# Performance work log

Hardware: AMD Instinct MI355X
Metric: run time of the kernel (lower is better)

## Reference

```python
import math
import jax, jax.numpy as jnp
import numpy as np

BSZ, N_HEADS, N_KV_HEADS, SEQLEN, HEAD_DIM = 1, 32, 8, 2048, 128
DIM = N_HEADS * HEAD_DIM  # 4096
N_REP = N_HEADS // N_KV_HEADS  # 4
NEG = -1e9


def setup_inputs() -> dict:
    key = jax.random.key(0)
    kq, kk, kv = jax.random.split(key, 3)
    q = jax.random.normal(kq, (BSZ, N_HEADS, SEQLEN, HEAD_DIM), dtype=jnp.float32)
    k = jax.random.normal(kk, (BSZ, N_KV_HEADS, SEQLEN, HEAD_DIM), dtype=jnp.float32)
    v = jax.random.normal(kv, (BSZ, N_KV_HEADS, SEQLEN, HEAD_DIM), dtype=jnp.float32)
    # additive causal mask: 0 on/below diagonal, large negative above
    causal = jnp.tril(jnp.ones((SEQLEN, SEQLEN), dtype=bool))
    mask = jnp.where(causal, 0.0, NEG).astype(jnp.float32)
    input_pos = jnp.zeros((1,), dtype=jnp.int64)
    return {"input_pos": input_pos, "q": q, "k": k, "v": v,
            "bsz": BSZ, "seqlen": SEQLEN, "mask": mask}


def reference(input_pos, q, k, v, bsz, seqlen, mask):
    # repeat_kv: (b, n_kv, s, d) -> (b, n_kv*n_rep, s, d), repeat_interleave on head dim
    k = jnp.repeat(k, N_REP, axis=1)
    v = jnp.repeat(v, N_REP, axis=1)
    scale = 1.0 / math.sqrt(q.shape[-1])
    # (b, h, s, s)
    attn = jnp.einsum("bhqd,bhkd->bhqk", q, k) * scale + mask
    attn = jax.nn.softmax(attn, axis=-1)
    y = jnp.einsum("bhqk,bhkd->bhqd", attn, v)  # (b, h, s, d)
    return y.transpose(0, 2, 1, 3).reshape(bsz, seqlen, DIM)
```

## Files before the change

kernel.cpp:

```cpp
#include <hip/hip_runtime.h>
#include <hip/hip_bf16.h>

#define SEQ 2048
#define HD 128
#define NH 32
#define NKV 8
#define ODIM 4096
#define QB 64
#define KVB 64
#define SCALE 0.08838834764831845f
#define SCALE_L2E 0.12752767f
#define NEGBIG -1e9f
#define NEGBIG_L2 -1.4426950e9f
#define THR_L2 11.54f

typedef __attribute__((ext_vector_type(8))) short bf16x8;
typedef __attribute__((ext_vector_type(4))) float f32x4;

__device__ __forceinline__ unsigned short f2bf(float x) {
  union { __hip_bfloat16 b; unsigned short u; } c;
  c.b = __float2bfloat16(x);
  return c.u;
}

__device__ __forceinline__ unsigned pack2bf(float lo, float hi) {
  union { __hip_bfloat162 h; unsigned u; } c;
  c.h = __float22bfloat162_rn(float2{lo, hi});
  return c.u;
}

__device__ __forceinline__ void gload_lds16(const unsigned char* g, unsigned char* l) {
  __builtin_amdgcn_global_load_lds(
      (const __attribute__((address_space(1))) void*)g,
      (__attribute__((address_space(3))) void*)l, 16, 0, 0);
}

#define KWORK (NKV * SEQ * 16)
#define VWORK (NKV * (SEQ / 2) * 16)
__global__ __launch_bounds__(256) void sdpa_prepass(
    const float* __restrict__ k, const float* __restrict__ v,
    unsigned char* __restrict__ ws) {
  unsigned char* kimg = ws;
  unsigned char* vimg = ws + (NKV * 32 * 16384);
  int idx = (int)blockIdx.x * 256 + (int)threadIdx.x;
  if (idx < KWORK) {
    int hkv = idx >> 15;
    int rem = idx & 32767;
    int rg = rem >> 4;
    int c8 = (rem & 15) << 3;
    const float* src = k + ((size_t)hkv * SEQ + rg) * HD + c8;
    float4 a = *(const float4*)(src);
    float4 b = *(const float4*)(src + 4);
    union { unsigned short hh[8]; uint4 u4; } pk;
    pk.hh[0]=f2bf(a.x); pk.hh[1]=f2bf(a.y); pk.hh[2]=f2bf(a.z); pk.hh[3]=f2bf(a.w);
    pk.hh[4]=f2bf(b.x); pk.hh[5]=f2bf(b.y); pk.hh[6]=f2bf(b.z); pk.hh[7]=f2bf(b.w);
    int t = rg >> 6, r = rg & 63;
    size_t base = ((size_t)(hkv * 32 + t)) << 14;
    *(uint4*)(kimg + base + (r << 8) + ((c8 << 1) ^ ((r & 7) << 4))) = pk.u4;
  } else {
    int u = idx - KWORK;
    if (u >= VWORK) return;
    int hkv = u >> 14;
    int rem = u & 16383;
    int pr = rem >> 4;
    int d0 = (rem & 15) << 3;
    int rg = pr << 1;
    const float* s0 = v + ((size_t)hkv * SEQ + rg) * HD + d0;
    const float* s1 = s0 + HD;
    float4 a0 = *(const float4*)(s0);
    float4 b0 = *(const float4*)(s0 + 4);
    float4 a1 = *(const float4*)(s1);
    float4 b1 = *(const float4*)(s1 + 4);
    float lo[8] = {a0.x,a0.y,a0.z,a0.w,b0.x,b0.y,b0.z,b0.w};
    float hi[8] = {a1.x,a1.y,a1.z,a1.w,b1.x,b1.y,b1.z,b1.w};
    int t = rg >> 6, rr = rg & 63;
    size_t base = ((size_t)(hkv * 32 + t)) << 14;
    int rb = rr << 1;
    #pragma unroll
    for (int j = 0; j < 8; ++j) {
      int d = d0 + j;
      *(unsigned*)(vimg + base + (d << 7) + (rb ^ ((d & 7) << 4))) =
          pack2bf(lo[j], hi[j]);
    }
  }
}

__global__ __launch_bounds__(512, 4) void sdpa_flash_kernel(
    const float* __restrict__ q, const unsigned char* __restrict__ kimg,
    const unsigned char* __restrict__ vimg, float* __restrict__ out) {
  __shared__ __align__(16) unsigned char smem[49152];
  const int tid = threadIdx.x;
  const int w = tid >> 6;
  const int l = tid & 63;
  const int lm = l & 15;
  const int lg = l >> 4;

  const int p = (int)blockIdx.x;
  const int qtA = p;
  const int qtB = 31 - p;
  const int myqt = (w < 4) ? qtA : qtB;
  const int h = (int)blockIdx.y;
  const int hkv = h >> 2;
  const int qbase = myqt * QB + 16 * (w & 3);
  const int myrow = qbase + lm;

  bf16x8 qa[4];
  {
    const float* qr = q + ((size_t)(h * SEQ + myrow)) * HD + 8 * lg;
    #pragma unroll
    for (int c = 0; c < 4; ++c) {
      float4 a = *(const float4*)(qr + 32 * c);
      float4 b = *(const float4*)(qr + 32 * c + 4);
      union { unsigned short hh[8]; bf16x8 vv; } pk;
      pk.hh[0] = f2bf(a.x * SCALE_L2E); pk.hh[1] = f2bf(a.y * SCALE_L2E);
      pk.hh[2] = f2bf(a.z * SCALE_L2E); pk.hh[3] = f2bf(a.w * SCALE_L2E);
      pk.hh[4] = f2bf(b.x * SCALE_L2E); pk.hh[5] = f2bf(b.y * SCALE_L2E);
      pk.hh[6] = f2bf(b.z * SCALE_L2E); pk.hh[7] = f2bf(b.w * SCALE_L2E);
      qa[c] = pk.vv;
    }
  }

  f32x4 o[8];
  #pragma unroll
  for (int i = 0; i < 8; ++i) o[i] = (f32x4){0.f, 0.f, 0.f, 0.f};
  float mrow = -1e30f;
  float lrow = 0.f;

  const int ntiles = qtB + 1;
  const unsigned char* kt0 = kimg + (((size_t)(hkv * 32)) << 14);
  const unsigned char* vt0 = vimg + (((size_t)(hkv * 32)) << 14);
  const int woff = w << 10;

#define STAGE_K(tt, Kb) {                                                    \
    const unsigned char* ks_ = kt0 + (((size_t)(tt)) << 14);                 \
    gload_lds16(ks_ + woff + (l << 4), (Kb) + woff);                         \
    gload_lds16(ks_ + 8192 + woff + (l << 4), (Kb) + 8192 + woff);           \
  }
#define STAGE_V(tt, Vb) {                                                    \
    const unsigned char* vs_ = vt0 + (((size_t)(tt)) << 14);                 \
    gload_lds16(vs_ + woff + (l << 4), (Vb) + woff);                         \
    gload_lds16(vs_ + 8192 + woff + (l << 4), (Vb) + 8192 + woff);           \
  }

  unsigned char* sA = smem;
  unsigned char* sB = smem + 16384;
  unsigned char* sC = smem + 32768;

  STAGE_K(0, sA);
  STAGE_V(0, sB);
  __syncthreads();

  for (int t = 0; t < ntiles; ++t) {
    const int kv0 = t * KVB;
    const bool have_next = (t + 1 < ntiles);
    if (have_next) STAGE_K(t + 1, sC);

    const bool act = (t <= myqt);
    bf16x8 pb[2];
    if (act) {
      f32x4 s[4];
      #pragma unroll
      for (int nt = 0; nt < 4; ++nt) s[nt] = (f32x4){0.f, 0.f, 0.f, 0.f};
      __builtin_amdgcn_s_setprio(1);
      #pragma unroll
      for (int nt = 0; nt < 4; ++nt) {
        int r = (nt << 4) + lm;
        #pragma unroll
        for (int kc = 0; kc < 4; ++kc) {
          int byte = (r << 8) + (((kc << 6) + (lg << 4)) ^ ((r & 7) << 4));
          bf16x8 kb = *(const bf16x8*)(sA + byte);
          s[nt] = __builtin_amdgcn_mfma_f32_16x16x32_bf16(kb, qa[kc], s[nt], 0, 0, 0);
        }
      }
      __builtin_amdgcn_s_setprio(0);

      if (kv0 + KVB - 1 > qbase) {
        #pragma unroll
        for (int nt = 0; nt < 4; ++nt) {
          #pragma unroll
          for (int i = 0; i < 4; ++i) {
            int col = kv0 + (nt << 4) + (lg << 2) + i;
            s[nt][i] += (col > myrow) ? NEGBIG_L2 : 0.f;
          }
        }
      }

      float tm = -1e30f;
      #pragma unroll
      for (int nt = 0; nt < 4; ++nt)
        #pragma unroll
        for (int i = 0; i < 4; ++i) tm = fmaxf(tm, s[nt][i]);
      tm = fmaxf(tm, __shfl_xor(tm, 16));
      tm = fmaxf(tm, __shfl_xor(tm, 32));
      if (!__all(tm <= mrow + THR_L2)) {
        float mn = fmaxf(mrow, tm);
        float fac = __builtin_amdgcn_exp2f(mrow - mn);
        mrow = mn;
        lrow *= fac;
        #pragma unroll
        for (int nt2 = 0; nt2 < 8; ++nt2) {
          #pragma unroll
          for (int i = 0; i < 4; ++i) o[nt2][i] *= fac;
        }
      }
      float rs = 0.f;
      #pragma unroll
      for (int nt = 0; nt < 4; ++nt) {
        #pragma unroll
        for (int i = 0; i < 4; ++i) {
          float pv = __builtin_amdgcn_exp2f(s[nt][i] - mrow);
          s[nt][i] = pv;
          rs += pv;
        }
      }
      rs += __shfl_xor(rs, 16);
      rs += __shfl_xor(rs, 32);
      lrow += rs;

      unsigned pk0[4], pk1[4];
      #pragma unroll
      for (int nt = 0; nt < 4; ++nt) {
        pk0[nt] = pack2bf(s[nt][0], s[nt][1]);
        pk1[nt] = pack2bf(s[nt][2], s[nt][3]);
      }
      const int srcA = lm + ((lg & 1) << 5);
      const int srcB = srcA + 16;
      const bool lo2 = (lg < 2);
      #pragma unroll
      for (int kc = 0; kc < 2; ++kc) {
        int a0 = __shfl((int)pk0[2*kc], srcA), b0 = __shfl((int)pk0[2*kc+1], srcA);
        int a1 = __shfl((int)pk1[2*kc], srcA), b1 = __shfl((int)pk1[2*kc+1], srcA);
        int a2 = __shfl((int)pk0[2*kc], srcB), b2 = __shfl((int)pk0[2*kc+1], srcB);
        int a3 = __shfl((int)pk1[2*kc], srcB), b3 = __shfl((int)pk1[2*kc+1], srcB);
        union { int uu[4]; bf16x8 v; } pw;
        pw.uu[0] = lo2 ? a0 : b0;
        pw.uu[1] = lo2 ? a1 : b1;
        pw.uu[2] = lo2 ? a2 : b2;
        pw.uu[3] = lo2 ? a3 : b3;
        pb[kc] = pw.v;
      }
    }

    __syncthreads();
    if (have_next) STAGE_V(t + 1, sA);

    if (act) {
      __builtin_amdgcn_s_setprio(1);
      #pragma unroll
      for (int nt2 = 0; nt2 < 8; ++nt2) {
        int dr = (nt2 << 4) + lm;
        #pragma unroll
        for (int kc = 0; kc < 2; ++kc) {
          int byte = (dr << 7) + (((kc << 6) + (lg << 4)) ^ ((dr & 7) << 4));
          bf16x8 vb = *(const bf16x8*)(sB + byte);
          o[nt2] = __builtin_amdgcn_mfma_f32_16x16x32_bf16(vb, pb[kc], o[nt2], 0, 0, 0);
        }
      }
      __builtin_amdgcn_s_setprio(0);
    }

    __syncthreads();
    unsigned char* nA = sC;
    unsigned char* nB = sA;
    unsigned char* nC = sB;
    sA = nA; sB = nB; sC = nC;
  }

  float inv = 1.f / lrow;
  float* orow = out + (size_t)myrow * ODIM + h * HD + (lg << 2);
  #pragma unroll
  for (int nt2 = 0; nt2 < 8; ++nt2) {
    float4 st = {o[nt2][0] * inv, o[nt2][1] * inv, o[nt2][2] * inv, o[nt2][3] * inv};
    *(float4*)(orow + (nt2 << 4)) = st;
  }
#undef STAGE_K
#undef STAGE_V
}

__global__ __launch_bounds__(512, 4) void sdpa_flash_fb(
    const float* __restrict__ q, const float* __restrict__ k,
    const float* __restrict__ v, float* __restrict__ out) {
  __shared__ __align__(16) unsigned char smem[65536];
  const int tid = threadIdx.x;
  const int w = tid >> 6;
  const int l = tid & 63;
  const int lm = l & 15;
  const int lg = l >> 4;
  const int p = (int)blockIdx.x;
  const int qtA = p;
  const int qtB = 31 - p;
  const int myqt = (w < 4) ? qtA : qtB;
  const int h = (int)blockIdx.y;
  const int hkv = h >> 2;
  const int qbase = myqt * QB + 16 * (w & 3);
  const int myrow = qbase + lm;
  bf16x8 qa[4];
  {
    const float* qr = q + ((size_t)(h * SEQ + myrow)) * HD + 8 * lg;
    #pragma unroll
    for (int c = 0; c < 4; ++c) {
      float4 a = *(const float4*)(qr + 32 * c);
      float4 b = *(const float4*)(qr + 32 * c + 4);
      union { unsigned short hh[8]; bf16x8 vv; } pk;
      pk.hh[0] = f2bf(a.x * SCALE); pk.hh[1] = f2bf(a.y * SCALE);
      pk.hh[2] = f2bf(a.z * SCALE); pk.hh[3] = f2bf(a.w * SCALE);
      pk.hh[4] = f2bf(b.x * SCALE); pk.hh[5] = f2bf(b.y * SCALE);
      pk.hh[6] = f2bf(b.z * SCALE); pk.hh[7] = f2bf(b.w * SCALE);
      qa[c] = pk.vv;
    }
  }
  f32x4 o[8];
  #pragma unroll
  for (int i = 0; i < 8; ++i) o[i] = (f32x4){0.f, 0.f, 0.f, 0.f};
  float mrow = -1e30f;
  float lrow = 0.f;
  const int ntiles = qtB + 1;
  const float* kg0 = k + (size_t)hkv * SEQ * HD;
  const float* vg0 = v + (size_t)hkv * SEQ * HD;
  const int k_r0 = tid >> 4;
  const int k_c8 = (tid & 15) << 3;
  const int v_rr = (tid & 31) << 1;
  const int v_d0 = (tid >> 5) << 3;
  float4 ka0, kb0, ka1, kb1, va0, vb0, va1, vb1;
#define LOADT(tt) {                                                          \
    const float* kg_ = kg0 + (size_t)((tt) * KVB) * HD + k_r0 * HD + k_c8;   \
    ka0 = *(const float4*)(kg_);                                             \
    kb0 = *(const float4*)(kg_ + 4);                                         \
    ka1 = *(const float4*)(kg_ + 32 * HD);                                   \
    kb1 = *(const float4*)(kg_ + 32 * HD + 4);                               \
    const float* vg_ = vg0 + (size_t)((tt) * KVB) * HD + v_rr * HD + v_d0;   \
    va0 = *(const float4*)(vg_);                                             \
    vb0 = *(const float4*)(vg_ + 4);                                         \
    va1 = *(const float4*)(vg_ + HD);                                        \
    vb1 = *(const float4*)(vg_ + HD + 4);                                    \
  }
#define WRITELDS(bufbase) {                                                  \
    unsigned char* Kb_ = (bufbase);                                          \
    unsigned char* Vb_ = (bufbase) + 16384;                                  \
    {                                                                        \
      union { unsigned short hh[8]; uint4 u4; } pk_;                         \
      pk_.hh[0]=f2bf(ka0.x); pk_.hh[1]=f2bf(ka0.y);                          \
      pk_.hh[2]=f2bf(ka0.z); pk_.hh[3]=f2bf(ka0.w);                          \
      pk_.hh[4]=f2bf(kb0.x); pk_.hh[5]=f2bf(kb0.y);                          \
      pk_.hh[6]=f2bf(kb0.z); pk_.hh[7]=f2bf(kb0.w);                          \
      int byte_ = (k_r0 << 8) + ((k_c8 << 1) ^ ((k_r0 & 7) << 4));           \
      *(uint4*)(Kb_ + byte_) = pk_.u4;                                       \
    }                                                                        \
    {                                                                        \
      int r1_ = k_r0 + 32;                                                   \
      union { unsigned short hh[8]; uint4 u4; } pk_;                         \
      pk_.hh[0]=f2bf(ka1.x); pk_.hh[1]=f2bf(ka1.y);                          \
      pk_.hh[2]=f2bf(ka1.z); pk_.hh[3]=f2bf(ka1.w);                          \
      pk_.hh[4]=f2bf(kb1.x); pk_.hh[5]=f2bf(kb1.y);                          \
      pk_.hh[6]=f2bf(kb1.z); pk_.hh[7]=f2bf(kb1.w);                          \
      int byte_ = (r1_ << 8) + ((k_c8 << 1) ^ ((r1_ & 7) << 4));             \
      *(uint4*)(Kb_ + byte_) = pk_.u4;                                       \
    }                                                                        \
    {                                                                        \
      unsigned w0_ = pack2bf(va0.x, va1.x), w1_ = pack2bf(va0.y, va1.y);     \
      unsigned w2_ = pack2bf(va0.z, va1.z), w3_ = pack2bf(va0.w, va1.w);     \
      unsigned w4_ = pack2bf(vb0.x, vb1.x), w5_ = pack2bf(vb0.y, vb1.y);     \
      unsigned w6_ = pack2bf(vb0.z, vb1.z), w7_ = pack2bf(vb0.w, vb1.w);     \
      int rb_ = v_rr << 1;                                                   \
      int d_;                                                                \
      d_ = v_d0;     *(unsigned*)(Vb_ + (d_ << 7) + (rb_ ^ ((d_ & 7) << 4))) = w0_; \
      d_ = v_d0 + 1; *(unsigned*)(Vb_ + (d_ << 7) + (rb_ ^ ((d_ & 7) << 4))) = w1_; \
      d_ = v_d0 + 2; *(unsigned*)(Vb_ + (d_ << 7) + (rb_ ^ ((d_ & 7) << 4))) = w2_; \
      d_ = v_d0 + 3; *(unsigned*)(Vb_ + (d_ << 7) + (rb_ ^ ((d_ & 7) << 4))) = w3_; \
      d_ = v_d0 + 4; *(unsigned*)(Vb_ + (d_ << 7) + (rb_ ^ ((d_ & 7) << 4))) = w4_; \
      d_ = v_d0 + 5; *(unsigned*)(Vb_ + (d_ << 7) + (rb_ ^ ((d_ & 7) << 4))) = w5_; \
      d_ = v_d0 + 6; *(unsigned*)(Vb_ + (d_ << 7) + (rb_ ^ ((d_ & 7) << 4))) = w6_; \
      d_ = v_d0 + 7; *(unsigned*)(Vb_ + (d_ << 7) + (rb_ ^ ((d_ & 7) << 4))) = w7_; \
    }                                                                        \
  }
  LOADT(0);
  WRITELDS(smem);
  __syncthreads();
  int cur = 0;
  for (int t = 0; t < ntiles; ++t) {
    const int kv0 = t * KVB;
    const bool have_next = (t + 1 < ntiles);
    if (have_next) LOADT(t + 1);
    unsigned char* Klds = smem + (cur << 15);
    unsigned char* Vlds = Klds + 16384;
    if (t <= myqt) {
      f32x4 s[4];
      #pragma unroll
      for (int nt = 0; nt < 4; ++nt) s[nt] = (f32x4){0.f, 0.f, 0.f, 0.f};
      #pragma unroll
      for (int nt = 0; nt < 4; ++nt) {
        int r = (nt << 4) + lm;
        #pragma unroll
        for (int kc = 0; kc < 4; ++kc) {
          int byte = (r << 8) + (((kc << 6) + (lg << 4)) ^ ((r & 7) << 4));
          bf16x8 kb = *(const bf16x8*)(Klds + byte);
          s[nt] = __builtin_amdgcn_mfma_f32_16x16x32_bf16(kb, qa[kc], s[nt], 0, 0, 0);
        }
      }
      if (kv0 + KVB - 1 > qbase) {
        #pragma unroll
        for (int nt = 0; nt < 4; ++nt) {
          #pragma unroll
          for (int i = 0; i < 4; ++i) {
            int col = kv0 + (nt << 4) + (lg << 2) + i;
            s[nt][i] += (col > myrow) ? NEGBIG : 0.f;
          }
        }
      }
      float tm = -1e30f;
      #pragma unroll
      for (int nt = 0; nt < 4; ++nt)
        #pragma unroll
        for (int i = 0; i < 4; ++i) tm = fmaxf(tm, s[nt][i]);
      tm = fmaxf(tm, __shfl_xor(tm, 16));
      tm = fmaxf(tm, __shfl_xor(tm, 32));
      float mn = fmaxf(mrow, tm);
      float fac = __expf(mrow - mn);
      mrow = mn;
      float rs = 0.f;
      #pragma unroll
      for (int nt = 0; nt < 4; ++nt) {
        #pragma unroll
        for (int i = 0; i < 4; ++i) {
          float pv = __expf(s[nt][i] - mn);
          s[nt][i] = pv;
          rs += pv;
        }
      }
      rs += __shfl_xor(rs, 16);
      rs += __shfl_xor(rs, 32);
      lrow = lrow * fac + rs;
      #pragma unroll
      for (int nt2 = 0; nt2 < 8; ++nt2) {
        #pragma unroll
        for (int i = 0; i < 4; ++i) o[nt2][i] *= fac;
      }
      unsigned pk0[4], pk1[4];
      #pragma unroll
      for (int nt = 0; nt < 4; ++nt) {
        pk0[nt] = pack2bf(s[nt][0], s[nt][1]);
        pk1[nt] = pack2bf(s[nt][2], s[nt][3]);
      }
      const int srcA = lm + ((lg & 1) << 5);
      const int srcB = srcA + 16;
      const bool lo2 = (lg < 2);
      bf16x8 pb[2];
      #pragma unroll
      for (int kc = 0; kc < 2; ++kc) {
        int a0 = __shfl((int)pk0[2*kc], srcA), b0 = __shfl((int)pk0[2*kc+1], srcA);
        int a1 = __shfl((int)pk1[2*kc], srcA), b1 = __shfl((int)pk1[2*kc+1], srcA);
        int a2 = __shfl((int)pk0[2*kc], srcB), b2 = __shfl((int)pk0[2*kc+1], srcB);
        int a3 = __shfl((int)pk1[2*kc], srcB), b3 = __shfl((int)pk1[2*kc+1], srcB);
        union { int uu[4]; bf16x8 v; } pw;
        pw.uu[0] = lo2 ? a0 : b0;
        pw.uu[1] = lo2 ? a1 : b1;
        pw.uu[2] = lo2 ? a2 : b2;
        pw.uu[3] = lo2 ? a3 : b3;
        pb[kc] = pw.v;
      }
      #pragma unroll
      for (int nt2 = 0; nt2 < 8; ++nt2) {
        int dr = (nt2 << 4) + lm;
        #pragma unroll
        for (int kc = 0; kc < 2; ++kc) {
          int byte = (dr << 7) + (((kc << 6) + (lg << 4)) ^ ((dr & 7) << 4));
          bf16x8 vb = *(const bf16x8*)(Vlds + byte);
          o[nt2] = __builtin_amdgcn_mfma_f32_16x16x32_bf16(vb, pb[kc], o[nt2], 0, 0, 0);
        }
      }
    }
    if (have_next) {
      WRITELDS(smem + ((cur ^ 1) << 15));
    }
    __syncthreads();
    cur ^= 1;
  }
  float inv = 1.f / lrow;
  float* orow = out + (size_t)myrow * ODIM + h * HD + (lg << 2);
  #pragma unroll
  for (int nt2 = 0; nt2 < 8; ++nt2) {
    float4 st = {o[nt2][0] * inv, o[nt2][1] * inv, o[nt2][2] * inv, o[nt2][3] * inv};
    *(float4*)(orow + (nt2 << 4)) = st;
  }
#undef LOADT
#undef WRITELDS
}

extern "C" void kernel_launch(void* const* d_in, const int* in_sizes, int n_in,
                              void* d_out, int out_size, void* d_ws, size_t ws_size,
                              hipStream_t stream) {
  const float* q = (const float*)d_in[1];
  const float* k = (const float*)d_in[2];
  const float* v = (const float*)d_in[3];
  float* out = (float*)d_out;
  dim3 grid(SEQ / QB / 2, NH);
  const size_t need = (size_t)(NKV * 32 * 16384) * 2;
  if (ws_size >= need && d_ws != nullptr) {
    unsigned char* ws = (unsigned char*)d_ws;
    int total = KWORK + VWORK;
    sdpa_prepass<<<(total + 255) / 256, 256, 0, stream>>>(k, v, ws);
    sdpa_flash_kernel<<<grid, 512, 0, stream>>>(
        q, ws, ws + (NKV * 32 * 16384), out);
  } else {
    sdpa_flash_fb<<<grid, 512, 0, stream>>>(q, k, v, out);
  }
}
```

Measured before the change: 82.67 us.

## Have each wave process both paired query tiles, halving block size to 256 threads

Each block previously used 8 waves, with 4 waves on query tile A and 4 on the mirrored tile B. Now 4 waves each handle 16 rows from both tiles. Every K/V fragment read from LDS feeds two MFMAs, which halves LDS read traffic per MFMA and removes the load imbalance where tile-A waves idled on later iterations. The cost is double the accumulator and Q registers per thread, lower launch bounds (256,2) with possibly fewer resident waves, and each wave issuing 4 async copies per stage instead of 2.

```diff
diff --git a/kernel.cpp b/kernel.cpp
--- a/kernel.cpp
+++ b/kernel.cpp
@@ -85,7 +85,7 @@
   }
 }
 
-__global__ __launch_bounds__(512, 4) void sdpa_flash_kernel(
+__global__ __launch_bounds__(256, 2) void sdpa_flash_kernel(
     const float* __restrict__ q, const unsigned char* __restrict__ kimg,
     const unsigned char* __restrict__ vimg, float* __restrict__ out) {
   __shared__ __align__(16) unsigned char smem[49152];
@@ -98,48 +98,61 @@
   const int p = (int)blockIdx.x;
   const int qtA = p;
   const int qtB = 31 - p;
-  const int myqt = (w < 4) ? qtA : qtB;
   const int h = (int)blockIdx.y;
   const int hkv = h >> 2;
-  const int qbase = myqt * QB + 16 * (w & 3);
-  const int myrow = qbase + lm;
-
-  bf16x8 qa[4];
+  const int qbaseA = qtA * QB + 16 * w;
+  const int qbaseB = qtB * QB + 16 * w;
+  const int rowA = qbaseA + lm;
+  const int rowB = qbaseB + lm;
+
+  bf16x8 qa[2][4];
   {
-    const float* qr = q + ((size_t)(h * SEQ + myrow)) * HD + 8 * lg;
+    const int rows2[2] = {rowA, rowB};
     #pragma unroll
-    for (int c = 0; c < 4; ++c) {
-      float4 a = *(const float4*)(qr + 32 * c);
-      float4 b = *(const float4*)(qr + 32 * c + 4);
-      union { unsigned short hh[8]; bf16x8 vv; } pk;
-      pk.hh[0] = f2bf(a.x * SCALE_L2E); pk.hh[1] = f2bf(a.y * SCALE_L2E);
-      pk.hh[2] = f2bf(a.z * SCALE_L2E); pk.hh[3] = f2bf(a.w * SCALE_L2E);
-      pk.hh[4] = f2bf(b.x * SCALE_L2E); pk.hh[5] = f2bf(b.y * SCALE_L2E);
-      pk.hh[6] = f2bf(b.z * SCALE_L2E); pk.hh[7] = f2bf(b.w * SCALE_L2E);
-      qa[c] = pk.vv;
-    }
-  }
-
-  f32x4 o[8];
+    for (int u = 0; u < 2; ++u) {
+      const float* qr = q + ((size_t)(h * SEQ + rows2[u])) * HD + 8 * lg;
+      #pragma unroll
+      for (int c = 0; c < 4; ++c) {
+        float4 a = *(const float4*)(qr + 32 * c);
+        float4 b = *(const float4*)(qr + 32 * c + 4);
+        union { unsigned short hh[8]; bf16x8 vv; } pk;
+        pk.hh[0] = f2bf(a.x * SCALE_L2E); pk.hh[1] = f2bf(a.y * SCALE_L2E);
+        pk.hh[2] = f2bf(a.z * SCALE_L2E); pk.hh[3] = f2bf(a.w * SCALE_L2E);
+        pk.hh[4] = f2bf(b.x * SCALE_L2E); pk.hh[5] = f2bf(b.y * SCALE_L2E);
+        pk.hh[6] = f2bf(b.z * SCALE_L2E); pk.hh[7] = f2bf(b.w * SCALE_L2E);
+        qa[u][c] = pk.vv;
+      }
+    }
+  }
+
+  f32x4 o[2][8];
   #pragma unroll
-  for (int i = 0; i < 8; ++i) o[i] = (f32x4){0.f, 0.f, 0.f, 0.f};
-  float mrow = -1e30f;
-  float lrow = 0.f;
+  for (int u = 0; u < 2; ++u)
+    #pragma unroll
+    for (int i = 0; i < 8; ++i) o[u][i] = (f32x4){0.f, 0.f, 0.f, 0.f};
+  float mrow[2] = {-1e30f, -1e30f};
+  float lrow[2] = {0.f, 0.f};
 
   const int ntiles = qtB + 1;
   const unsigned char* kt0 = kimg + (((size_t)(hkv * 32)) << 14);
   const unsigned char* vt0 = vimg + (((size_t)(hkv * 32)) << 14);
-  const int woff = w << 10;
+  const int woff = w << 12;
 
 #define STAGE_K(tt, Kb) {                                                    \
-    const unsigned char* ks_ = kt0 + (((size_t)(tt)) << 14);                 \
-    gload_lds16(ks_ + woff + (l << 4), (Kb) + woff);                         \
-    gload_lds16(ks_ + 8192 + woff + (l << 4), (Kb) + 8192 + woff);           \
+    const unsigned char* ks_ = kt0 + (((size_t)(tt)) << 14) + woff + (l << 4); \
+    unsigned char* kd_ = (Kb) + woff;                                        \
+    gload_lds16(ks_, kd_);                                                   \
+    gload_lds16(ks_ + 1024, kd_ + 1024);                                     \
+    gload_lds16(ks_ + 2048, kd_ + 2048);                                     \
+    gload_lds16(ks_ + 3072, kd_ + 3072);                                     \
   }
 #define STAGE_V(tt, Vb) {                                                    \
-    const unsigned char* vs_ = vt0 + (((size_t)(tt)) << 14);                 \
-    gload_lds16(vs_ + woff + (l << 4), (Vb) + woff);                         \
-    gload_lds16(vs_ + 8192 + woff + (l << 4), (Vb) + 8192 + woff);           \
+    const unsigned char* vs_ = vt0 + (((size_t)(tt)) << 14) + woff + (l << 4); \
+    unsigned char* vd_ = (Vb) + woff;                                        \
+    gload_lds16(vs_, vd_);                                                   \
+    gload_lds16(vs_ + 1024, vd_ + 1024);                                     \
+    gload_lds16(vs_ + 2048, vd_ + 2048);                                     \
+    gload_lds16(vs_ + 3072, vd_ + 3072);                                     \
   }
 
   unsigned char* sA = smem;
@@ -155,12 +168,16 @@
     const bool have_next = (t + 1 < ntiles);
     if (have_next) STAGE_K(t + 1, sC);
 
-    const bool act = (t <= myqt);
-    bf16x8 pb[2];
-    if (act) {
-      f32x4 s[4];
-      #pragma unroll
-      for (int nt = 0; nt < 4; ++nt) s[nt] = (f32x4){0.f, 0.f, 0.f, 0.f};
+    const bool actA = (t <= qtA);
+    f32x4 s[2][4];
+    bf16x8 pb[2][2];
+
+    if (actA) {
+      #pragma unroll
+      for (int nt = 0; nt < 4; ++nt) {
+        s[0][nt] = (f32x4){0.f, 0.f, 0.f, 0.f};
+        s[1][nt] = (f32x4){0.f, 0.f, 0.f, 0.f};
+      }
       __builtin_amdgcn_s_setprio(1);
       #pragma unroll
       for (int nt = 0; nt < 4; ++nt) {
@@ -169,59 +186,86 @@
         for (int kc = 0; kc < 4; ++kc) {
           int byte = (r << 8) + (((kc << 6) + (lg << 4)) ^ ((r & 7) << 4));
           bf16x8 kb = *(const bf16x8*)(sA + byte);
-          s[nt] = __builtin_amdgcn_mfma_f32_16x16x32_bf16(kb, qa[kc], s[nt], 0, 0, 0);
+          s[0][nt] = __builtin_amdgcn_mfma_f32_16x16x32_bf16(kb, qa[0][kc], s[0][nt], 0, 0, 0);
+          s[1][nt] = __builtin_amdgcn_mfma_f32_16x16x32_bf16(kb, qa[1][kc], s[1][nt], 0, 0, 0);
         }
       }
       __builtin_amdgcn_s_setprio(0);
-
-      if (kv0 + KVB - 1 > qbase) {
-        #pragma unroll
-        for (int nt = 0; nt < 4; ++nt) {
-          #pragma unroll
-          for (int i = 0; i < 4; ++i) {
-            int col = kv0 + (nt << 4) + (lg << 2) + i;
-            s[nt][i] += (col > myrow) ? NEGBIG_L2 : 0.f;
-          }
-        }
-      }
-
+    } else {
+      #pragma unroll
+      for (int nt = 0; nt < 4; ++nt) s[1][nt] = (f32x4){0.f, 0.f, 0.f, 0.f};
+      __builtin_amdgcn_s_setprio(1);
+      #pragma unroll
+      for (int nt = 0; nt < 4; ++nt) {
+        int r = (nt << 4) + lm;
+        #pragma unroll
+        for (int kc = 0; kc < 4; ++kc) {
+          int byte = (r << 8) + (((kc << 6) + (lg << 4)) ^ ((r & 7) << 4));
+          bf16x8 kb = *(const bf16x8*)(sA + byte);
+          s[1][nt] = __builtin_amdgcn_mfma_f32_16x16x32_bf16(kb, qa[1][kc], s[1][nt], 0, 0, 0);
+        }
+      }
+      __builtin_amdgcn_s_setprio(0);
+    }
+
+    if (t == qtA) {
+      #pragma unroll
+      for (int nt = 0; nt < 4; ++nt)
+        #pragma unroll
+        for (int i = 0; i < 4; ++i) {
+          int col = kv0 + (nt << 4) + (lg << 2) + i;
+          s[0][nt][i] += (col > rowA) ? NEGBIG_L2 : 0.f;
+        }
+    }
+    if (t == qtB) {
+      #pragma unroll
+      for (int nt = 0; nt < 4; ++nt)
+        #pragma unroll
+        for (int i = 0; i < 4; ++i) {
+          int col = kv0 + (nt << 4) + (lg << 2) + i;
+          s[1][nt][i] += (col > rowB) ? NEGBIG_L2 : 0.f;
+        }
+    }
+
+    #pragma unroll
+    for (int u = 0; u < 2; ++u) {
+      if (u == 0 && !actA) continue;
       float tm = -1e30f;
       #pragma unroll
       for (int nt = 0; nt < 4; ++nt)
         #pragma unroll
-        for (int i = 0; i < 4; ++i) tm = fmaxf(tm, s[nt][i]);
+        for (int i = 0; i < 4; ++i) tm = fmaxf(tm, s[u][nt][i]);
       tm = fmaxf(tm, __shfl_xor(tm, 16));
       tm = fmaxf(tm, __shfl_xor(tm, 32));
-      if (!__all(tm <= mrow + THR_L2)) {
-        float mn = fmaxf(mrow, tm);
-        float fac = __builtin_amdgcn_exp2f(mrow - mn);
-        mrow = mn;
-        lrow *= fac;
-        #pragma unroll
-        for (int nt2 = 0; nt2 < 8; ++nt2) {
+      if (!__all(tm <= mrow[u] + THR_L2)) {
+        float mn = fmaxf(mrow[u], tm);
+        float fac = __builtin_amdgcn_exp2f(mrow[u] - mn);
+        mrow[u] = mn;
+        lrow[u] *= fac;
+        #pragma unroll
+        for (int nt2 = 0; nt2 < 8; ++nt2)
           #pragma unroll
-          for (int i = 0; i < 4; ++i) o[nt2][i] *= fac;
-        }
+          for (int i = 0; i < 4; ++i) o[u][nt2][i] *= fac;
       }
       float rs = 0.f;
       #pragma unroll
       for (int nt = 0; nt < 4; ++nt) {
         #pragma unroll
         for (int i = 0; i < 4; ++i) {
-          float pv = __builtin_amdgcn_exp2f(s[nt][i] - mrow);
-          s[nt][i] = pv;
+          float pv = __builtin_amdgcn_exp2f(s[u][nt][i] - mrow[u]);
+          s[u][nt][i] = pv;
           rs += pv;
         }
       }
       rs += __shfl_xor(rs, 16);
       rs += __shfl_xor(rs, 32);
-      lrow += rs;
+      lrow[u] += rs;
 
       unsigned pk0[4], pk1[4];
       #pragma unroll
       for (int nt = 0; nt < 4; ++nt) {
-        pk0[nt] = pack2bf(s[nt][0], s[nt][1]);
-        pk1[nt] = pack2bf(s[nt][2], s[nt][3]);
+        pk0[nt] = pack2bf(s[u][nt][0], s[u][nt][1]);
+        pk1[nt] = pack2bf(s[u][nt][2], s[u][nt][3]);
       }
       const int srcA = lm + ((lg & 1) << 5);
       const int srcB = srcA + 16;
@@ -237,14 +281,14 @@
         pw.uu[1] = lo2 ? a1 : b1;
         pw.uu[2] = lo2 ? a2 : b2;
         pw.uu[3] = lo2 ? a3 : b3;
-        pb[kc] = pw.v;
+        pb[u][kc] = pw.v;
       }
     }
 
     __syncthreads();
     if (have_next) STAGE_V(t + 1, sA);
 
-    if (act) {
+    if (actA) {
       __builtin_amdgcn_s_setprio(1);
       #pragma unroll
       for (int nt2 = 0; nt2 < 8; ++nt2) {
@@ -253,7 +297,21 @@
         for (int kc = 0; kc < 2; ++kc) {
           int byte = (dr << 7) + (((kc << 6) + (lg << 4)) ^ ((dr & 7) << 4));
           bf16x8 vb = *(const bf16x8*)(sB + byte);
-          o[nt2] = __builtin_amdgcn_mfma_f32_16x16x32_bf16(vb, pb[kc], o[nt2], 0, 0, 0);
+          o[0][nt2] = __builtin_amdgcn_mfma_f32_16x16x32_bf16(vb, pb[0][kc], o[0][nt2], 0, 0, 0);
+          o[1][nt2] = __builtin_amdgcn_mfma_f32_16x16x32_bf16(vb, pb[1][kc], o[1][nt2], 0, 0, 0);
+        }
+      }
+      __builtin_amdgcn_s_setprio(0);
+    } else {
+      __builtin_amdgcn_s_setprio(1);
+      #pragma unroll
+      for (int nt2 = 0; nt2 < 8; ++nt2) {
+        int dr = (nt2 << 4) + lm;
+        #pragma unroll
+        for (int kc = 0; kc < 2; ++kc) {
+          int byte = (dr << 7) + (((kc << 6) + (lg << 4)) ^ ((dr & 7) << 4));
+          bf16x8 vb = *(const bf16x8*)(sB + byte);
+          o[1][nt2] = __builtin_amdgcn_mfma_f32_16x16x32_bf16(vb, pb[1][kc], o[1][nt2], 0, 0, 0);
         }
       }
       __builtin_amdgcn_s_setprio(0);
@@ -266,12 +324,19 @@
     sA = nA; sB = nB; sC = nC;
   }
 
-  float inv = 1.f / lrow;
-  float* orow = out + (size_t)myrow * ODIM + h * HD + (lg << 2);
-  #pragma unroll
-  for (int nt2 = 0; nt2 < 8; ++nt2) {
-    float4 st = {o[nt2][0] * inv, o[nt2][1] * inv, o[nt2][2] * inv, o[nt2][3] * inv};
-    *(float4*)(orow + (nt2 << 4)) = st;
+  {
+    const int rows2[2] = {rowA, rowB};
+    #pragma unroll
+    for (int u = 0; u < 2; ++u) {
+      float inv = 1.f / lrow[u];
+      float* orow = out + (size_t)rows2[u] * ODIM + h * HD + (lg << 2);
+      #pragma unroll
+      for (int nt2 = 0; nt2 < 8; ++nt2) {
+        float4 st = {o[u][nt2][0] * inv, o[u][nt2][1] * inv,
+                     o[u][nt2][2] * inv, o[u][nt2][3] * inv};
+        *(float4*)(orow + (nt2 << 4)) = st;
+      }
+    }
   }
 #undef STAGE_K
 #undef STAGE_V
@@ -493,15 +558,16 @@
   const float* k = (const float*)d_in[2];
   const float* v = (const float*)d_in[3];
   float* out = (float*)d_out;
-  dim3 grid(SEQ / QB / 2, NH);
   const size_t need = (size_t)(NKV * 32 * 16384) * 2;
   if (ws_size >= need && d_ws != nullptr) {
     unsigned char* ws = (unsigned char*)d_ws;
     int total = KWORK + VWORK;
     sdpa_prepass<<<(total + 255) / 256, 256, 0, stream>>>(k, v, ws);
-    sdpa_flash_kernel<<<grid, 512, 0, stream>>>(
+    dim3 grid(SEQ / QB / 2, NH);
+    sdpa_flash_kernel<<<grid, 256, 0, stream>>>(
         q, ws, ws + (NKV * 32 * 16384), out);
   } else {
-    sdpa_flash_fb<<<grid, 512, 0, stream>>>(q, k, v, out);
-  }
-}
+    dim3 gridf(SEQ / QB / 2, NH);
+    sdpa_flash_fb<<<gridf, 512, 0, stream>>>(q, k, v, out);
+  }
+}
```

New measurement: 87.74 us. +6.1%, slower.

## Replace paired causal q-tile blocks with one q-tile per 256-thread block

Applied to the files above, without the earlier changes.

The main flash kernel stops pairing q-tile p with q-tile 31-p inside one 512-thread block. Each block now runs 4 waves on a single 64-row q-tile, with the grid doubled and blocks ordered heaviest first. This removes the idle waves of the short half, which waited at barriers while the long half ran, and drops the per-tile active check. The costs are that load balance now depends on the hardware scheduler handling uneven causal blocks, and each wave issues four LDS staging loads per tile instead of two.

```diff
diff --git a/kernel.cpp b/kernel.cpp
--- a/kernel.cpp
+++ b/kernel.cpp
@@ -85,7 +85,7 @@
   }
 }
 
-__global__ __launch_bounds__(512, 4) void sdpa_flash_kernel(
+__global__ __launch_bounds__(256, 4) void sdpa_flash_kernel(
     const float* __restrict__ q, const unsigned char* __restrict__ kimg,
     const unsigned char* __restrict__ vimg, float* __restrict__ out) {
   __shared__ __align__(16) unsigned char smem[49152];
@@ -95,13 +95,10 @@
   const int lm = l & 15;
   const int lg = l >> 4;
 
-  const int p = (int)blockIdx.x;
-  const int qtA = p;
-  const int qtB = 31 - p;
-  const int myqt = (w < 4) ? qtA : qtB;
+  const int qt = 31 - (int)blockIdx.x;
   const int h = (int)blockIdx.y;
   const int hkv = h >> 2;
-  const int qbase = myqt * QB + 16 * (w & 3);
+  const int qbase = qt * QB + 16 * w;
   const int myrow = qbase + lm;
 
   bf16x8 qa[4];
@@ -126,20 +123,26 @@
   float mrow = -1e30f;
   float lrow = 0.f;
 
-  const int ntiles = qtB + 1;
+  const int ntiles = qt + 1;
   const unsigned char* kt0 = kimg + (((size_t)(hkv * 32)) << 14);
   const unsigned char* vt0 = vimg + (((size_t)(hkv * 32)) << 14);
-  const int woff = w << 10;
+  const int woff = w << 12;
 
 #define STAGE_K(tt, Kb) {                                                    \
-    const unsigned char* ks_ = kt0 + (((size_t)(tt)) << 14);                 \
-    gload_lds16(ks_ + woff + (l << 4), (Kb) + woff);                         \
-    gload_lds16(ks_ + 8192 + woff + (l << 4), (Kb) + 8192 + woff);           \
+    const unsigned char* ks_ = kt0 + (((size_t)(tt)) << 14) + woff + (l << 4); \
+    unsigned char* kd_ = (Kb) + woff;                                        \
+    gload_lds16(ks_, kd_);                                                   \
+    gload_lds16(ks_ + 1024, kd_ + 1024);                                     \
+    gload_lds16(ks_ + 2048, kd_ + 2048);                                     \
+    gload_lds16(ks_ + 3072, kd_ + 3072);                                     \
   }
 #define STAGE_V(tt, Vb) {                                                    \
-    const unsigned char* vs_ = vt0 + (((size_t)(tt)) << 14);                 \
-    gload_lds16(vs_ + woff + (l << 4), (Vb) + woff);                         \
-    gload_lds16(vs_ + 8192 + woff + (l << 4), (Vb) + 8192 + woff);           \
+    const unsigned char* vs_ = vt0 + (((size_t)(tt)) << 14) + woff + (l << 4); \
+    unsigned char* vd_ = (Vb) + woff;                                        \
+    gload_lds16(vs_, vd_);                                                   \
+    gload_lds16(vs_ + 1024, vd_ + 1024);                                     \
+    gload_lds16(vs_ + 2048, vd_ + 2048);                                     \
+    gload_lds16(vs_ + 3072, vd_ + 3072);                                     \
   }
 
   unsigned char* sA = smem;
@@ -155,109 +158,104 @@
     const bool have_next = (t + 1 < ntiles);
     if (have_next) STAGE_K(t + 1, sC);
 
-    const bool act = (t <= myqt);
+    f32x4 s[4];
+    #pragma unroll
+    for (int nt = 0; nt < 4; ++nt) s[nt] = (f32x4){0.f, 0.f, 0.f, 0.f};
+    __builtin_amdgcn_s_setprio(1);
+    #pragma unroll
+    for (int nt = 0; nt < 4; ++nt) {
+      int r = (nt << 4) + lm;
+      #pragma unroll
+      for (int kc = 0; kc < 4; ++kc) {
+        int byte = (r << 8) + (((kc << 6) + (lg << 4)) ^ ((r & 7) << 4));
+        bf16x8 kb = *(const bf16x8*)(sA + byte);
+        s[nt] = __builtin_amdgcn_mfma_f32_16x16x32_bf16(kb, qa[kc], s[nt], 0, 0, 0);
+      }
+    }
+    __builtin_amdgcn_s_setprio(0);
+
+    if (t == qt) {
+      #pragma unroll
+      for (int nt = 0; nt < 4; ++nt) {
+        #pragma unroll
+        for (int i = 0; i < 4; ++i) {
+          int col = kv0 + (nt << 4) + (lg << 2) + i;
+          s[nt][i] += (col > myrow) ? NEGBIG_L2 : 0.f;
+        }
+      }
+    }
+
+    float tm = -1e30f;
+    #pragma unroll
+    for (int nt = 0; nt < 4; ++nt)
+      #pragma unroll
+      for (int i = 0; i < 4; ++i) tm = fmaxf(tm, s[nt][i]);
+    tm = fmaxf(tm, __shfl_xor(tm, 16));
+    tm = fmaxf(tm, __shfl_xor(tm, 32));
+    if (!__all(tm <= mrow + THR_L2)) {
+      float mn = fmaxf(mrow, tm);
+      float fac = __builtin_amdgcn_exp2f(mrow - mn);
+      mrow = mn;
+      lrow *= fac;
+      #pragma unroll
+      for (int nt2 = 0; nt2 < 8; ++nt2) {
+        #pragma unroll
+        for (int i = 0; i < 4; ++i) o[nt2][i] *= fac;
+      }
+    }
+    float rs = 0.f;
+    #pragma unroll
+    for (int nt = 0; nt < 4; ++nt) {
+      #pragma unroll
+      for (int i = 0; i < 4; ++i) {
+        float pv = __builtin_amdgcn_exp2f(s[nt][i] - mrow);
+        s[nt][i] = pv;
+        rs += pv;
+      }
+    }
+    rs += __shfl_xor(rs, 16);
+    rs += __shfl_xor(rs, 32);
+    lrow += rs;
+
+    unsigned pk0[4], pk1[4];
+    #pragma unroll
+    for (int nt = 0; nt < 4; ++nt) {
+      pk0[nt] = pack2bf(s[nt][0], s[nt][1]);
+      pk1[nt] = pack2bf(s[nt][2], s[nt][3]);
+    }
+    const int srcA = lm + ((lg & 1) << 5);
+    const int srcB = srcA + 16;
+    const bool lo2 = (lg < 2);
     bf16x8 pb[2];
-    if (act) {
-      f32x4 s[4];
-      #pragma unroll
-      for (int nt = 0; nt < 4; ++nt) s[nt] = (f32x4){0.f, 0.f, 0.f, 0.f};
-      __builtin_amdgcn_s_setprio(1);
-      #pragma unroll
-      for (int nt = 0; nt < 4; ++nt) {
-        int r = (nt << 4) + lm;
-        #pragma unroll
-        for (int kc = 0; kc < 4; ++kc) {
-          int byte = (r << 8) + (((kc << 6) + (lg << 4)) ^ ((r & 7) << 4));
-          bf16x8 kb = *(const bf16x8*)(sA + byte);
-          s[nt] = __builtin_amdgcn_mfma_f32_16x16x32_bf16(kb, qa[kc], s[nt], 0, 0, 0);
-        }
-      }
-      __builtin_amdgcn_s_setprio(0);
-
-      if (kv0 + KVB - 1 > qbase) {
-        #pragma unroll
-        for (int nt = 0; nt < 4; ++nt) {
-          #pragma unroll
-          for (int i = 0; i < 4; ++i) {
-            int col = kv0 + (nt << 4) + (lg << 2) + i;
-            s[nt][i] += (col > myrow) ? NEGBIG_L2 : 0.f;
-          }
-        }
-      }
-
-      float tm = -1e30f;
-      #pragma unroll
-      for (int nt = 0; nt < 4; ++nt)
-        #pragma unroll
-        for (int i = 0; i < 4; ++i) tm = fmaxf(tm, s[nt][i]);
-      tm = fmaxf(tm, __shfl_xor(tm, 16));
-      tm = fmaxf(tm, __shfl_xor(tm, 32));
-      if (!__all(tm <= mrow + THR_L2)) {
-        float mn = fmaxf(mrow, tm);
-        float fac = __builtin_amdgcn_exp2f(mrow - mn);
-        mrow = mn;
-        lrow *= fac;
-        #pragma unroll
-        for (int nt2 = 0; nt2 < 8; ++nt2) {
-          #pragma unroll
-          for (int i = 0; i < 4; ++i) o[nt2][i] *= fac;
-        }
-      }
-      float rs = 0.f;
-      #pragma unroll
-      for (int nt = 0; nt < 4; ++nt) {
-        #pragma unroll
-        for (int i = 0; i < 4; ++i) {
-          float pv = __builtin_amdgcn_exp2f(s[nt][i] - mrow);
-          s[nt][i] = pv;
-          rs += pv;
-        }
-      }
-      rs += __shfl_xor(rs, 16);
-      rs += __shfl_xor(rs, 32);
-      lrow += rs;
-
-      unsigned pk0[4], pk1[4];
-      #pragma unroll
-      for (int nt = 0; nt < 4; ++nt) {
-        pk0[nt] = pack2bf(s[nt][0], s[nt][1]);
-        pk1[nt] = pack2bf(s[nt][2], s[nt][3]);
-      }
-      const int srcA = lm + ((lg & 1) << 5);
-      const int srcB = srcA + 16;
-      const bool lo2 = (lg < 2);
-      #pragma unroll
-      for (int kc = 0; kc < 2; ++kc) {
-        int a0 = __shfl((int)pk0[2*kc], srcA), b0 = __shfl((int)pk0[2*kc+1], srcA);
-        int a1 = __shfl((int)pk1[2*kc], srcA), b1 = __shfl((int)pk1[2*kc+1], srcA);
-        int a2 = __shfl((int)pk0[2*kc], srcB), b2 = __shfl((int)pk0[2*kc+1], srcB);
-        int a3 = __shfl((int)pk1[2*kc], srcB), b3 = __shfl((int)pk1[2*kc+1], srcB);
-        union { int uu[4]; bf16x8 v; } pw;
-        pw.uu[0] = lo2 ? a0 : b0;
-        pw.uu[1] = lo2 ? a1 : b1;
-        pw.uu[2] = lo2 ? a2 : b2;
-        pw.uu[3] = lo2 ? a3 : b3;
-        pb[kc] = pw.v;
-      }
+    #pragma unroll
+    for (int kc = 0; kc < 2; ++kc) {
+      int a0 = __shfl((int)pk0[2*kc], srcA), b0 = __shfl((int)pk0[2*kc+1], srcA);
+      int a1 = __shfl((int)pk1[2*kc], srcA), b1 = __shfl((int)pk1[2*kc+1], srcA);
+      int a2 = __shfl((int)pk0[2*kc], srcB), b2 = __shfl((int)pk0[2*kc+1], srcB);
+      int a3 = __shfl((int)pk1[2*kc], srcB), b3 = __shfl((int)pk1[2*kc+1], srcB);
+      union { int uu[4]; bf16x8 v; } pw;
+      pw.uu[0] = lo2 ? a0 : b0;
+      pw.uu[1] = lo2 ? a1 : b1;
+      pw.uu[2] = lo2 ? a2 : b2;
+      pw.uu[3] = lo2 ? a3 : b3;
+      pb[kc] = pw.v;
     }
 
     __syncthreads();
     if (have_next) STAGE_V(t + 1, sA);
 
-    if (act) {
-      __builtin_amdgcn_s_setprio(1);
-      #pragma unroll
-      for (int nt2 = 0; nt2 < 8; ++nt2) {
-        int dr = (nt2 << 4) + lm;
-        #pragma unroll
-        for (int kc = 0; kc < 2; ++kc) {
-          int byte = (dr << 7) + (((kc << 6) + (lg << 4)) ^ ((dr & 7) << 4));
-          bf16x8 vb = *(const bf16x8*)(sB + byte);
-          o[nt2] = __builtin_amdgcn_mfma_f32_16x16x32_bf16(vb, pb[kc], o[nt2], 0, 0, 0);
-        }
-      }
-      __builtin_amdgcn_s_setprio(0);
-    }
+    __builtin_amdgcn_s_setprio(1);
+    #pragma unroll
+    for (int nt2 = 0; nt2 < 8; ++nt2) {
+      int dr = (nt2 << 4) + lm;
+      #pragma unroll
+      for (int kc = 0; kc < 2; ++kc) {
+        int byte = (dr << 7) + (((kc << 6) + (lg << 4)) ^ ((dr & 7) << 4));
+        bf16x8 vb = *(const bf16x8*)(sB + byte);
+        o[nt2] = __builtin_amdgcn_mfma_f32_16x16x32_bf16(vb, pb[kc], o[nt2], 0, 0, 0);
+      }
+    }
+    __builtin_amdgcn_s_setprio(0);
 
     __syncthreads();
     unsigned char* nA = sC;
@@ -493,15 +491,16 @@
   const float* k = (const float*)d_in[2];
   const float* v = (const float*)d_in[3];
   float* out = (float*)d_out;
-  dim3 grid(SEQ / QB / 2, NH);
   const size_t need = (size_t)(NKV * 32 * 16384) * 2;
   if (ws_size >= need && d_ws != nullptr) {
     unsigned char* ws = (unsigned char*)d_ws;
     int total = KWORK + VWORK;
     sdpa_prepass<<<(total + 255) / 256, 256, 0, stream>>>(k, v, ws);
-    sdpa_flash_kernel<<<grid, 512, 0, stream>>>(
+    dim3 grid(SEQ / QB, NH);
+    sdpa_flash_kernel<<<grid, 256, 0, stream>>>(
         q, ws, ws + (NKV * 32 * 16384), out);
   } else {
-    sdpa_flash_fb<<<grid, 512, 0, stream>>>(q, k, v, out);
-  }
-}
+    dim3 gridf(SEQ / QB / 2, NH);
+    sdpa_flash_fb<<<gridf, 512, 0, stream>>>(q, k, v, out);
+  }
+}
```

After: 137.1 us. +65.8%, slower.
